# Kernel tuning notes

Measured on AMD Instinct MI355X. Metric: run time of the kernel, lower is better.

## Reference

```python
import jax, jax.numpy as jnp
import numpy as np

FP8_MAX = 448.0  # float8_e4m3fn max
NUM_HEADS = 16

def _fp8_quant_dequant(t):
    # per-(batch, head) symmetric scaling into fp8 e4m3 range, cast to fp8 and back
    amax = jnp.max(jnp.abs(t), axis=(-2, -1), keepdims=True)
    scale = FP8_MAX / jnp.maximum(amax, 1e-12)
    t8 = (t * scale).astype(jnp.float8_e4m3fn).astype(t.dtype)
    return t8 / scale

def setup_inputs() -> dict:
    key = jax.random.key(0)
    k1, k2, k3 = jax.random.split(key, 3)
    B, N, C = 2, 2048, 1024
    x = jax.random.normal(k1, (B, N, C), dtype=jnp.float32)
    w_qkv = jax.random.normal(k2, (C, 3 * C), dtype=jnp.float32) * (C ** -0.5)
    w_proj = jax.random.normal(k3, (C, C), dtype=jnp.float32) * (C ** -0.5)
    b_proj = jnp.zeros((C,), dtype=jnp.float32)
    return {"x": x, "w_qkv": w_qkv, "w_proj": w_proj, "b_proj": b_proj}

def reference(x, w_qkv, w_proj, b_proj):
    B, N, C = x.shape
    H = NUM_HEADS
    D = C // H
    scale = D ** -0.5
    qkv = (x @ w_qkv).reshape(B, N, 3, H, D).transpose(2, 0, 3, 1, 4)  # [3,B,H,N,D]
    q, k, v = qkv[0], qkv[1], qkv[2]
    # sage-style fp8 quantize/dequant of q and k fused into score computation
    q = _fp8_quant_dequant(q)
    k = _fp8_quant_dequant(k)
    scores = jnp.einsum('bhqd,bhkd->bhqk', q, k) * scale  # [B,H,N,N]
    causal = jnp.tril(jnp.ones((N, N), dtype=bool))
    scores = jnp.where(causal[None, None], scores, jnp.finfo(scores.dtype).min)
    attn = jax.nn.softmax(scores, axis=-1)
    out = jnp.einsum('bhqk,bhkd->bhqd', attn, v)  # [B,H,N,D]
    out = out.transpose(0, 2, 1, 3).reshape(B, N, C)
    return out @ w_proj + b_proj
```

## Files before the change

kernel.cpp:

```cpp
#include <hip/hip_runtime.h>

#define B_   2
#define N_   2048
#define C_   1024
#define H_   16
#define D_   64
#define BH_  (B_*H_)
#define NDH  (N_*D_)
#define M1   (B_*N_)

typedef __attribute__((ext_vector_type(4))) float    f32x4;
typedef __attribute__((ext_vector_type(8))) _Float16 f16x8;
typedef __attribute__((ext_vector_type(4))) _Float16 f16x4;

#define GLOAD_LDS(gp, lp) \
  __builtin_amdgcn_global_load_lds((const __attribute__((address_space(1))) void*)(gp), \
                                   (__attribute__((address_space(3))) void*)(lp), 16, 0, 0)

__global__ void k_cvt16(const float* __restrict__ in, _Float16* __restrict__ out, int n4) {
  int i = blockIdx.x * blockDim.x + threadIdx.x;
  if (i >= n4) return;
  float4 v = ((const float4*)in)[i];
  f16x4 o;
  o.x = (_Float16)v.x; o.y = (_Float16)v.y; o.z = (_Float16)v.z; o.w = (_Float16)v.w;
  ((f16x4*)out)[i] = o;
}

__global__ __launch_bounds__(256) void k_transmerge(const float* __restrict__ wq,
                                                    const float* __restrict__ wp,
                                                    _Float16* __restrict__ whT,
                                                    _Float16* __restrict__ wpT,
                                                    unsigned* __restrict__ amax_u) {
  if (blockIdx.x == 0 && threadIdx.x < 64) amax_u[threadIdx.x] = 0u;
  __shared__ _Float16 t[64][68];
  int idx = blockIdx.x;
  const float* in; _Float16* out; int Cc, cx, cy;
  if (idx < 768) { in = wq; out = whT; Cc = 3072; cx = idx % 48; cy = idx / 48; }
  else { idx -= 768; in = wp; out = wpT; Cc = 1024; cx = idx % 16; cy = idx / 16; }
  const int R = 1024;
  int c0 = cx * 64, r0 = cy * 64;
  int tid = threadIdx.x;
  int cq = tid & 15, rq = tid >> 4;
#pragma unroll
  for (int i = 0; i < 4; ++i) {
    int r = rq + i * 16;
    float4 v = *(const float4*)(in + (size_t)(r0 + r) * Cc + c0 + cq * 4);
    t[r][cq*4+0] = (_Float16)v.x;
    t[r][cq*4+1] = (_Float16)v.y;
    t[r][cq*4+2] = (_Float16)v.z;
    t[r][cq*4+3] = (_Float16)v.w;
  }
  __syncthreads();
#pragma unroll
  for (int i = 0; i < 4; ++i) {
    int c = rq + i * 16;
    f16x4 o;
    o.x = t[cq*4+0][c];
    o.y = t[cq*4+1][c];
    o.z = t[cq*4+2][c];
    o.w = t[cq*4+3][c];
    *(f16x4*)(out + (size_t)(c0 + c) * R + r0 + cq * 4) = o;
  }
}

__global__ __launch_bounds__(256) void k_gemm_qkv(const _Float16* __restrict__ A,
                                                  const _Float16* __restrict__ BT,
                                                  _Float16* __restrict__ qh,
                                                  _Float16* __restrict__ kh,
                                                  _Float16* __restrict__ vh,
                                                  unsigned* __restrict__ amax_u) {
  __shared__ __align__(16) _Float16 As[128 * 32];
  __shared__ __align__(16) _Float16 Bs[128 * 32];
  const int tid = threadIdx.x, lane = tid & 63, wave = tid >> 6;
  const int wm = wave >> 1, wn = wave & 1;
  const int mcol = lane & 15, quad = lane >> 4;
  const int m0 = blockIdx.x * 128, n0 = blockIdx.y * 128;
  f32x4 acc[4][4] = {};
  for (int k0 = 0; k0 < 1024; k0 += 32) {
#pragma unroll
    for (int r = 0; r < 2; ++r) {
      int c = tid + r * 256;
      int row = c >> 2, kc = c & 3;
      GLOAD_LDS(A  + (size_t)(m0 + row) * 1024 + k0 + kc * 8, &As[c * 8]);
      GLOAD_LDS(BT + (size_t)(n0 + row) * 1024 + k0 + kc * 8, &Bs[c * 8]);
    }
    __syncthreads();
    f16x8 af[4], bf[4];
#pragma unroll
    for (int tm = 0; tm < 4; ++tm)
      af[tm] = *(const f16x8*)&As[(wm * 64 + tm * 16 + mcol) * 32 + quad * 8];
#pragma unroll
    for (int tn = 0; tn < 4; ++tn)
      bf[tn] = *(const f16x8*)&Bs[(wn * 64 + tn * 16 + mcol) * 32 + quad * 8];
#pragma unroll
    for (int tm = 0; tm < 4; ++tm)
#pragma unroll
      for (int tn = 0; tn < 4; ++tn)
        acc[tm][tn] = __builtin_amdgcn_mfma_f32_16x16x32_f16(af[tm], bf[tn], acc[tm][tn], 0, 0, 0);
    __syncthreads();
  }
  const int sec = n0 >> 10;
  if (sec < 2) {
    _Float16* dst = sec ? kh : qh;
    float mxv = 0.f;
#pragma unroll
    for (int tm = 0; tm < 4; ++tm)
#pragma unroll
      for (int tn = 0; tn < 4; ++tn) {
        int rowb = m0 + wm * 64 + tm * 16 + quad * 4;
        int col = n0 + wn * 64 + tn * 16 + mcol;
        int cc = col & 1023, h = cc >> 6, d = cc & 63;
        int b = rowb >> 11, n = rowb & 2047;
        f32x4 a = acc[tm][tn];
        mxv = fmaxf(mxv, fmaxf(fmaxf(fabsf(a[0]), fabsf(a[1])),
                               fmaxf(fabsf(a[2]), fabsf(a[3]))));
        f16x4 o;
        o.x = (_Float16)a[0]; o.y = (_Float16)a[1];
        o.z = (_Float16)a[2]; o.w = (_Float16)a[3];
        *(f16x4*)&dst[(size_t)(b * 16 + h) * 131072 + (size_t)(n >> 5) * 2048 + d * 32 + (n & 31)] = o;
      }
#pragma unroll
    for (int off = 32; off; off >>= 1) mxv = fmaxf(mxv, __shfl_xor(mxv, off));
    if (lane == 0) {
      int head = ((n0 & 1023) >> 6) + wn;
      int plane = (m0 >> 11) * 16 + head;
      atomicMax(&amax_u[sec * 32 + plane], __float_as_uint(mxv));
    }
  } else {
#pragma unroll
    for (int tm = 0; tm < 4; ++tm)
#pragma unroll
      for (int tn = 0; tn < 4; ++tn) {
        int rowb = m0 + wm * 64 + tm * 16 + quad * 4;
        int col = n0 + wn * 64 + tn * 16 + mcol;
        int cc = col & 1023, h = cc >> 6, d = cc & 63;
        int b = rowb >> 11, n = rowb & 2047;
        f16x4 o;
        o.x = (_Float16)acc[tm][tn][0];
        o.y = (_Float16)acc[tm][tn][1];
        o.z = (_Float16)acc[tm][tn][2];
        o.w = (_Float16)acc[tm][tn][3];
        *(f16x4*)&vh[(size_t)(b * 16 + h) * 131072 + (size_t)(n >> 5) * 2048 + d * 32 + (n & 31)] = o;
      }
  }
}

__global__ __launch_bounds__(256) void k_quant(const _Float16* __restrict__ qh,
                                               const _Float16* __restrict__ kh,
                                               const float* __restrict__ amax,
                                               char* __restrict__ q8,
                                               char* __restrict__ k8) {
  __shared__ ushort T[32][72];
  int blk = blockIdx.x;
  int which = blk >> 11;
  int idx = blk & 2047;
  int bh = idx >> 6, chunk = idx & 63;
  const _Float16* src = (which ? kh : qh) + (size_t)bh * NDH + chunk * 2048;
  float s = 448.f / fmaxf(amax[which * 32 + bh], 1e-12f);
  int t = threadIdx.x;
  f16x8 v = *(const f16x8*)(src + t * 8);
  int d = t >> 2, kk0 = (t & 3) * 8;
#pragma unroll
  for (int j = 0; j < 8; ++j) T[kk0 + j][d] = ((const ushort*)&v)[j];
  __syncthreads();
  int r = t >> 3, d0 = (t & 7) * 8;
  f16x8 row = *(const f16x8*)&T[r][d0];
  float f[8];
#pragma unroll
  for (int j = 0; j < 8; ++j) f[j] = (float)((const _Float16*)&row)[j] * s;
  int lo = 0, hi = 0;
  lo = __builtin_amdgcn_cvt_pk_fp8_f32(f[0], f[1], lo, false);
  lo = __builtin_amdgcn_cvt_pk_fp8_f32(f[2], f[3], lo, true);
  hi = __builtin_amdgcn_cvt_pk_fp8_f32(f[4], f[5], hi, false);
  hi = __builtin_amdgcn_cvt_pk_fp8_f32(f[6], f[7], hi, true);
  int2 o; o.x = lo; o.y = hi;
  if (which == 0) {
    char* dst = q8 + (size_t)bh * NDH + (size_t)(chunk * 32 + r) * 64 + d0;
    *(int2*)dst = o;
  } else {
    int e = (r >> 2) & 1;
    int mc = (r >> 3) * 4 + (r & 3);
    int kb = d0 >> 5, dq = (d0 >> 3) & 3;
    char* dst = k8 + (size_t)bh * NDH + chunk * 2048 + (e * 2 + kb) * 512 + mc * 32 + dq * 8;
    *(int2*)dst = o;
  }
}

__global__ __launch_bounds__(256, 2) void k_flash(const char* __restrict__ q8,
                                                  const char* __restrict__ k8,
                                                  const _Float16* __restrict__ vh,
                                                  const float* __restrict__ amax,
                                                  _Float16* __restrict__ attn) {
  const int bh = blockIdx.x;
  const int wave = threadIdx.x >> 6, lane = threadIdx.x & 63;
  const int mcol = lane & 15, quad = lane >> 4;
  const int pr = blockIdx.y * 4 + wave;
  const int ga = pr, gb = 127 - pr;
  const int ta = (ga >> 3) + 1;

  float sq = 448.f / fmaxf(amax[bh], 1e-12f);
  float sk = 448.f / fmaxf(amax[32 + bh], 1e-12f);
  const float c2 = (1.f / (sq * sk)) * 0.125f * 1.44269504089f;

  const size_t pbase = (size_t)bh * NDH;
  const char* kbase = k8 + pbase + mcol * 32 + quad * 8;
  const _Float16* vbase = vh + pbase + mcol * 32 + quad * 8;
  const int qrowA = ga * 16 + mcol, qrowB = gb * 16 + mcol;
  long aqA0, aqA1, aqB0, aqB1;
  { const char* qp = q8 + pbase + (size_t)qrowA * 64;
    aqA0 = *(const long*)(qp + quad * 8); aqA1 = *(const long*)(qp + 32 + quad * 8); }
  { const char* qp = q8 + pbase + (size_t)qrowB * 64;
    aqB0 = *(const long*)(qp + quad * 8); aqB1 = *(const long*)(qp + 32 + quad * 8); }

  f32x4 O[4] = {};
  float m_i = -3e38f, l_i = 0.f;
  const int b = bh >> 4, h = bh & 15;
  const int kq = quad * 8;

  long kc[16], kn[16];
  {
    const char* kp = kbase;
#pragma unroll
    for (int i = 0; i < 16; ++i) kc[i] = *(const long*)(kp + i * 512);
  }

  auto body = [&](int t, long (&cur)[16], long (&nxt)[16]) {
    const bool inB = t >= ta;
    const int n0 = (inB ? t - ta : t) * 128;
    const long aq0 = inB ? aqB0 : aqA0;
    const long aq1 = inB ? aqB1 : aqA1;
    const int qrow = inB ? qrowB : qrowA;
    const bool last = inB ? (t == 16) : (t == ta - 1);

    f32x4 s[4][2];
#pragma unroll
    for (int p = 0; p < 4; ++p)
#pragma unroll
      for (int e = 0; e < 2; ++e) {
        f32x4 z = {};
        z = __builtin_amdgcn_mfma_f32_16x16x32_fp8_fp8(cur[p * 4 + e * 2 + 0], aq0, z, 0, 0, 0);
        z = __builtin_amdgcn_mfma_f32_16x16x32_fp8_fp8(cur[p * 4 + e * 2 + 1], aq1, z, 0, 0, 0);
        s[p][e] = z;
      }
    f16x8 va[4][4];
    {
      const _Float16* vp = vbase + (size_t)(n0 >> 5) * 2048;
#pragma unroll
      for (int p = 0; p < 4; ++p)
#pragma unroll
        for (int dt = 0; dt < 4; ++dt)
          va[dt][p] = *(const f16x8*)(vp + p * 2048 + dt * 512);
    }
    if (t < 16) {
      const int t2 = t + 1;
      const int n02 = ((t2 >= ta) ? t2 - ta : t2) * 128;
      const char* kp = kbase + (size_t)(n02 >> 5) * 2048;
#pragma unroll
      for (int i = 0; i < 16; ++i) nxt[i] = *(const long*)(kp + i * 512);
    }
    if (last) {
#pragma unroll
      for (int p = 0; p < 4; ++p)
#pragma unroll
        for (int e = 0; e < 2; ++e)
#pragma unroll
          for (int r = 0; r < 4; ++r) {
            int key = n0 + p * 32 + kq + e * 4 + r;
            float v = s[p][e][r] * c2;
            s[p][e][r] = (key <= qrow) ? v : -3e38f;
          }
    } else {
#pragma unroll
      for (int p = 0; p < 4; ++p)
#pragma unroll
        for (int e = 0; e < 2; ++e)
#pragma unroll
          for (int r = 0; r < 4; ++r)
            s[p][e][r] = s[p][e][r] * c2;
    }
    float fm[8];
#pragma unroll
    for (int p = 0; p < 4; ++p)
#pragma unroll
      for (int e = 0; e < 2; ++e) {
        f32x4 v = s[p][e];
        fm[p * 2 + e] = fmaxf(fmaxf(v[0], v[1]), fmaxf(v[2], v[3]));
      }
    float mx = fmaxf(fmaxf(fmaxf(fm[0], fm[1]), fmaxf(fm[2], fm[3])),
                     fmaxf(fmaxf(fm[4], fm[5]), fmaxf(fm[6], fm[7])));
    mx = fmaxf(mx, m_i);
    mx = fmaxf(mx, __shfl_xor(mx, 16));
    mx = fmaxf(mx, __shfl_xor(mx, 32));
    float alpha = exp2f(m_i - mx);
    m_i = mx;
    float fs[8];
#pragma unroll
    for (int p = 0; p < 4; ++p)
#pragma unroll
      for (int e = 0; e < 2; ++e) {
        float p0 = exp2f(s[p][e][0] - mx);
        float p1 = exp2f(s[p][e][1] - mx);
        float p2 = exp2f(s[p][e][2] - mx);
        float p3 = exp2f(s[p][e][3] - mx);
        s[p][e][0] = p0; s[p][e][1] = p1; s[p][e][2] = p2; s[p][e][3] = p3;
        fs[p * 2 + e] = (p0 + p1) + (p2 + p3);
      }
    float sum = ((fs[0] + fs[1]) + (fs[2] + fs[3])) + ((fs[4] + fs[5]) + (fs[6] + fs[7]));
    sum += __shfl_xor(sum, 16);
    sum += __shfl_xor(sum, 32);
    l_i = l_i * alpha + sum;
#pragma unroll
    for (int dt = 0; dt < 4; ++dt)
#pragma unroll
      for (int r = 0; r < 4; ++r)
        O[dt][r] *= alpha;
#pragma unroll
    for (int p = 0; p < 4; ++p) {
      f16x8 pb;
      pb[0] = (_Float16)s[p][0][0]; pb[1] = (_Float16)s[p][0][1];
      pb[2] = (_Float16)s[p][0][2]; pb[3] = (_Float16)s[p][0][3];
      pb[4] = (_Float16)s[p][1][0]; pb[5] = (_Float16)s[p][1][1];
      pb[6] = (_Float16)s[p][1][2]; pb[7] = (_Float16)s[p][1][3];
#pragma unroll
      for (int dt = 0; dt < 4; ++dt)
        O[dt] = __builtin_amdgcn_mfma_f32_16x16x32_f16(va[dt][p], pb, O[dt], 0, 0, 0);
    }
    if (last) {
      float rl = 1.f / l_i;
      _Float16* op = attn + ((size_t)b * 2048 + qrow) * 1024 + h * 64;
#pragma unroll
      for (int dt = 0; dt < 4; ++dt) {
        f16x4 o;
        o.x = (_Float16)(O[dt][0] * rl);
        o.y = (_Float16)(O[dt][1] * rl);
        o.z = (_Float16)(O[dt][2] * rl);
        o.w = (_Float16)(O[dt][3] * rl);
        *(f16x4*)(op + dt * 16 + quad * 4) = o;
        O[dt] = (f32x4){0.f, 0.f, 0.f, 0.f};
      }
      m_i = -3e38f; l_i = 0.f;
    }
  };

#pragma unroll 1
  for (int t = 0; t < 17; t += 2) {
    body(t, kc, kn);
    if (t + 1 < 17) body(t + 1, kn, kc);
  }
}

__global__ __launch_bounds__(256) void k_gemm_out(const _Float16* __restrict__ A,
                                                  const _Float16* __restrict__ BT,
                                                  const float* __restrict__ bias,
                                                  float* __restrict__ out) {
  __shared__ __align__(16) _Float16 As[128 * 32];
  __shared__ __align__(16) _Float16 Bs[128 * 32];
  const int tid = threadIdx.x, lane = tid & 63, wave = tid >> 6;
  const int wm = wave >> 1, wn = wave & 1;
  const int mcol = lane & 15, quad = lane >> 4;
  const int m0 = blockIdx.x * 128, n0 = blockIdx.y * 128;
  f32x4 acc[4][4] = {};
  for (int k0 = 0; k0 < 1024; k0 += 32) {
#pragma unroll
    for (int r = 0; r < 2; ++r) {
      int c = tid + r * 256;
      int row = c >> 2, kc = c & 3;
      GLOAD_LDS(A  + (size_t)(m0 + row) * 1024 + k0 + kc * 8, &As[c * 8]);
      GLOAD_LDS(BT + (size_t)(n0 + row) * 1024 + k0 + kc * 8, &Bs[c * 8]);
    }
    __syncthreads();
    f16x8 af[4], bf[4];
#pragma unroll
    for (int tm = 0; tm < 4; ++tm)
      af[tm] = *(const f16x8*)&As[(wm * 64 + tm * 16 + mcol) * 32 + quad * 8];
#pragma unroll
    for (int tn = 0; tn < 4; ++tn)
      bf[tn] = *(const f16x8*)&Bs[(wn * 64 + tn * 16 + mcol) * 32 + quad * 8];
#pragma unroll
    for (int tm = 0; tm < 4; ++tm)
#pragma unroll
      for (int tn = 0; tn < 4; ++tn)
        acc[tm][tn] = __builtin_amdgcn_mfma_f32_16x16x32_f16(af[tm], bf[tn], acc[tm][tn], 0, 0, 0);
    __syncthreads();
  }
#pragma unroll
  for (int tm = 0; tm < 4; ++tm)
#pragma unroll
    for (int tn = 0; tn < 4; ++tn)
#pragma unroll
      for (int reg = 0; reg < 4; ++reg) {
        int row = m0 + wm * 64 + tm * 16 + quad * 4 + reg;
        int col = n0 + wn * 64 + tn * 16 + mcol;
        out[(size_t)row * 1024 + col] = acc[tm][tn][reg] + bias[col];
      }
}

extern "C" void kernel_launch(void* const* d_in, const int* in_sizes, int n_in,
                              void* d_out, int out_size, void* d_ws, size_t ws_size,
                              hipStream_t stream) {
  const float* x      = (const float*)d_in[0];
  const float* w_qkv  = (const float*)d_in[1];
  const float* w_proj = (const float*)d_in[2];
  const float* b_proj = (const float*)d_in[3];
  float* out = (float*)d_out;

  char* ws = (char*)d_ws;
  _Float16* xh   = (_Float16*)ws; ws += (size_t)M1 * C_ * 2;
  _Float16* whT  = (_Float16*)ws; ws += (size_t)3 * C_ * C_ * 2;
  _Float16* wpT  = (_Float16*)ws; ws += (size_t)C_ * C_ * 2;
  _Float16* qh   = (_Float16*)ws; ws += (size_t)BH_ * NDH * 2;
  _Float16* kh   = (_Float16*)ws; ws += (size_t)BH_ * NDH * 2;
  _Float16* vh   = (_Float16*)ws; ws += (size_t)BH_ * NDH * 2;
  char*     q8   = (char*)ws;     ws += (size_t)BH_ * NDH;
  char*     k8   = (char*)ws;     ws += (size_t)BH_ * NDH;
  _Float16* attn = (_Float16*)ws; ws += (size_t)M1 * C_ * 2;
  float*    amx  = (float*)ws;    ws += 256;

  k_cvt16<<<(M1 * C_ / 4 + 255) / 256, 256, 0, stream>>>(x, xh, M1 * C_ / 4);
  k_transmerge<<<1024, 256, 0, stream>>>(w_qkv, w_proj, whT, wpT, (unsigned*)amx);
  k_gemm_qkv<<<dim3(M1 / 128, 3 * C_ / 128), 256, 0, stream>>>(xh, whT, qh, kh, vh, (unsigned*)amx);
  k_quant<<<4096, 256, 0, stream>>>(qh, kh, amx, q8, k8);
  k_flash<<<dim3(32, 16), 256, 0, stream>>>(q8, k8, vh, amx, attn);
  k_gemm_out<<<dim3(M1 / 128, C_ / 128), 256, 0, stream>>>(attn, wpT, b_proj, out);
}
```

Measured before the change: 215.4 us.

## Split each flash row-pair across two waves with LDS merge of partial softmax

The flash kernel now gives each pair of query tiles (A and B) to two waves instead of one. One wave does tile A plus the first part of tile B's keys, and the other does the rest of B's keys. The partial O, m and l are merged through shared memory. The grid doubles, launch bounds allow four blocks per CU, the score scale is folded into an fma before exp2, and P is packed with cvt_pkrtz. This aims to shorten the serial per-wave chain of 17 key tiles to 8–9 and raise occupancy, at the cost of LDS use, a __syncthreads, and more register pressure from the higher occupancy target.

```diff
diff --git a/kernel.cpp b/kernel.cpp
--- a/kernel.cpp
+++ b/kernel.cpp
@@ -12,6 +12,7 @@
 typedef __attribute__((ext_vector_type(4))) float    f32x4;
 typedef __attribute__((ext_vector_type(8))) _Float16 f16x8;
 typedef __attribute__((ext_vector_type(4))) _Float16 f16x4;
+typedef __attribute__((ext_vector_type(2))) __fp16   fp16v2;
 
 #define GLOAD_LDS(gp, lp) \
   __builtin_amdgcn_global_load_lds((const __attribute__((address_space(1))) void*)(gp), \
@@ -186,15 +187,18 @@
   }
 }
 
-__global__ __launch_bounds__(256, 2) void k_flash(const char* __restrict__ q8,
+__global__ __launch_bounds__(256, 4) void k_flash(const char* __restrict__ q8,
                                                   const char* __restrict__ k8,
                                                   const _Float16* __restrict__ vh,
                                                   const float* __restrict__ amax,
                                                   _Float16* __restrict__ attn) {
+  __shared__ float Osh[2][16][68];
+  __shared__ float Msh[2][16], Lsh[2][16];
   const int bh = blockIdx.x;
   const int wave = threadIdx.x >> 6, lane = threadIdx.x & 63;
   const int mcol = lane & 15, quad = lane >> 4;
-  const int pr = blockIdx.y * 4 + wave;
+  const int pi = wave >> 1, role = wave & 1;
+  const int pr = blockIdx.y * 2 + pi;
   const int ga = pr, gb = 127 - pr;
   const int ta = (ga >> 3) + 1;
 
@@ -206,31 +210,36 @@
   const char* kbase = k8 + pbase + mcol * 32 + quad * 8;
   const _Float16* vbase = vh + pbase + mcol * 32 + quad * 8;
   const int qrowA = ga * 16 + mcol, qrowB = gb * 16 + mcol;
-  long aqA0, aqA1, aqB0, aqB1;
-  { const char* qp = q8 + pbase + (size_t)qrowA * 64;
-    aqA0 = *(const long*)(qp + quad * 8); aqA1 = *(const long*)(qp + 32 + quad * 8); }
-  { const char* qp = q8 + pbase + (size_t)qrowB * 64;
-    aqB0 = *(const long*)(qp + quad * 8); aqB1 = *(const long*)(qp + 32 + quad * 8); }
+
+  long aq0v, aq1v;
+  { int qr = role ? qrowB : qrowA;
+    const char* qp = q8 + pbase + (size_t)qr * 64;
+    aq0v = *(const long*)(qp + quad * 8); aq1v = *(const long*)(qp + 32 + quad * 8); }
 
   f32x4 O[4] = {};
   float m_i = -3e38f, l_i = 0.f;
   const int b = bh >> 4, h = bh & 15;
   const int kq = quad * 8;
+  const int NT = role ? 8 : 9;
+
+  auto u_n0 = [&](int u) -> int {
+    if (role) return (9 - ta + u) << 7;
+    return (u < ta ? u : u - ta) << 7;
+  };
 
   long kc[16], kn[16];
   {
-    const char* kp = kbase;
+    const char* kp = kbase + (size_t)(u_n0(0) >> 5) * 2048;
 #pragma unroll
     for (int i = 0; i < 16; ++i) kc[i] = *(const long*)(kp + i * 512);
   }
 
-  auto body = [&](int t, long (&cur)[16], long (&nxt)[16]) {
-    const bool inB = t >= ta;
-    const int n0 = (inB ? t - ta : t) * 128;
-    const long aq0 = inB ? aqB0 : aqA0;
-    const long aq1 = inB ? aqB1 : aqA1;
-    const int qrow = inB ? qrowB : qrowA;
-    const bool last = inB ? (t == 16) : (t == ta - 1);
+  auto body = [&](int u, long (&cur)[16], long (&nxt)[16]) {
+    const bool inA = (!role) && (u < ta);
+    const int n0 = u_n0(u);
+    const int qrow = inA ? qrowA : qrowB;
+    const bool maskT = role ? (u == 7) : (u == ta - 1);
+    const bool emitA = (!role) && (u == ta - 1);
 
     f32x4 s[4][2];
 #pragma unroll
@@ -238,8 +247,8 @@
 #pragma unroll
       for (int e = 0; e < 2; ++e) {
         f32x4 z = {};
-        z = __builtin_amdgcn_mfma_f32_16x16x32_fp8_fp8(cur[p * 4 + e * 2 + 0], aq0, z, 0, 0, 0);
-        z = __builtin_amdgcn_mfma_f32_16x16x32_fp8_fp8(cur[p * 4 + e * 2 + 1], aq1, z, 0, 0, 0);
+        z = __builtin_amdgcn_mfma_f32_16x16x32_fp8_fp8(cur[p * 4 + e * 2 + 0], aq0v, z, 0, 0, 0);
+        z = __builtin_amdgcn_mfma_f32_16x16x32_fp8_fp8(cur[p * 4 + e * 2 + 1], aq1v, z, 0, 0, 0);
         s[p][e] = z;
       }
     f16x8 va[4][4];
@@ -251,14 +260,12 @@
         for (int dt = 0; dt < 4; ++dt)
           va[dt][p] = *(const f16x8*)(vp + p * 2048 + dt * 512);
     }
-    if (t < 16) {
-      const int t2 = t + 1;
-      const int n02 = ((t2 >= ta) ? t2 - ta : t2) * 128;
-      const char* kp = kbase + (size_t)(n02 >> 5) * 2048;
+    if (u + 1 < NT) {
+      const char* kp = kbase + (size_t)(u_n0(u + 1) >> 5) * 2048;
 #pragma unroll
       for (int i = 0; i < 16; ++i) nxt[i] = *(const long*)(kp + i * 512);
     }
-    if (last) {
+    if (maskT) {
 #pragma unroll
       for (int p = 0; p < 4; ++p)
 #pragma unroll
@@ -266,17 +273,8 @@
 #pragma unroll
           for (int r = 0; r < 4; ++r) {
             int key = n0 + p * 32 + kq + e * 4 + r;
-            float v = s[p][e][r] * c2;
-            s[p][e][r] = (key <= qrow) ? v : -3e38f;
+            s[p][e][r] = (key <= qrow) ? s[p][e][r] : -3e38f;
           }
-    } else {
-#pragma unroll
-      for (int p = 0; p < 4; ++p)
-#pragma unroll
-        for (int e = 0; e < 2; ++e)
-#pragma unroll
-          for (int r = 0; r < 4; ++r)
-            s[p][e][r] = s[p][e][r] * c2;
     }
     float fm[8];
 #pragma unroll
@@ -286,23 +284,25 @@
         f32x4 v = s[p][e];
         fm[p * 2 + e] = fmaxf(fmaxf(v[0], v[1]), fmaxf(v[2], v[3]));
       }
-    float mx = fmaxf(fmaxf(fmaxf(fm[0], fm[1]), fmaxf(fm[2], fm[3])),
+    float rm = fmaxf(fmaxf(fmaxf(fm[0], fm[1]), fmaxf(fm[2], fm[3])),
                      fmaxf(fmaxf(fm[4], fm[5]), fmaxf(fm[6], fm[7])));
-    mx = fmaxf(mx, m_i);
+    float mx = fmaxf(m_i, rm * c2);
     mx = fmaxf(mx, __shfl_xor(mx, 16));
     mx = fmaxf(mx, __shfl_xor(mx, 32));
     float alpha = exp2f(m_i - mx);
     m_i = mx;
     float fs[8];
+    union { f16x8 v8; fp16v2 v2[4]; } pb[4];
 #pragma unroll
     for (int p = 0; p < 4; ++p)
 #pragma unroll
       for (int e = 0; e < 2; ++e) {
-        float p0 = exp2f(s[p][e][0] - mx);
-        float p1 = exp2f(s[p][e][1] - mx);
-        float p2 = exp2f(s[p][e][2] - mx);
-        float p3 = exp2f(s[p][e][3] - mx);
-        s[p][e][0] = p0; s[p][e][1] = p1; s[p][e][2] = p2; s[p][e][3] = p3;
+        float p0 = exp2f(__builtin_fmaf(s[p][e][0], c2, -mx));
+        float p1 = exp2f(__builtin_fmaf(s[p][e][1], c2, -mx));
+        float p2 = exp2f(__builtin_fmaf(s[p][e][2], c2, -mx));
+        float p3 = exp2f(__builtin_fmaf(s[p][e][3], c2, -mx));
+        pb[p].v2[e * 2 + 0] = __builtin_amdgcn_cvt_pkrtz(p0, p1);
+        pb[p].v2[e * 2 + 1] = __builtin_amdgcn_cvt_pkrtz(p2, p3);
         fs[p * 2 + e] = (p0 + p1) + (p2 + p3);
       }
     float sum = ((fs[0] + fs[1]) + (fs[2] + fs[3])) + ((fs[4] + fs[5]) + (fs[6] + fs[7]));
@@ -315,19 +315,13 @@
       for (int r = 0; r < 4; ++r)
         O[dt][r] *= alpha;
 #pragma unroll
-    for (int p = 0; p < 4; ++p) {
-      f16x8 pb;
-      pb[0] = (_Float16)s[p][0][0]; pb[1] = (_Float16)s[p][0][1];
-      pb[2] = (_Float16)s[p][0][2]; pb[3] = (_Float16)s[p][0][3];
-      pb[4] = (_Float16)s[p][1][0]; pb[5] = (_Float16)s[p][1][1];
-      pb[6] = (_Float16)s[p][1][2]; pb[7] = (_Float16)s[p][1][3];
+    for (int p = 0; p < 4; ++p)
 #pragma unroll
       for (int dt = 0; dt < 4; ++dt)
-        O[dt] = __builtin_amdgcn_mfma_f32_16x16x32_f16(va[dt][p], pb, O[dt], 0, 0, 0);
-    }
-    if (last) {
+        O[dt] = __builtin_amdgcn_mfma_f32_16x16x32_f16(va[dt][p], pb[p].v8, O[dt], 0, 0, 0);
+    if (emitA) {
       float rl = 1.f / l_i;
-      _Float16* op = attn + ((size_t)b * 2048 + qrow) * 1024 + h * 64;
+      _Float16* op = attn + ((size_t)b * 2048 + qrowA) * 1024 + h * 64;
 #pragma unroll
       for (int dt = 0; dt < 4; ++dt) {
         f16x4 o;
@@ -339,13 +333,41 @@
         O[dt] = (f32x4){0.f, 0.f, 0.f, 0.f};
       }
       m_i = -3e38f; l_i = 0.f;
+      const char* qp = q8 + pbase + (size_t)qrowB * 64;
+      aq0v = *(const long*)(qp + quad * 8);
+      aq1v = *(const long*)(qp + 32 + quad * 8);
     }
   };
 
 #pragma unroll 1
-  for (int t = 0; t < 17; t += 2) {
-    body(t, kc, kn);
-    if (t + 1 < 17) body(t + 1, kn, kc);
+  for (int u = 0; u < NT; u += 2) {
+    body(u, kc, kn);
+    if (u + 1 < NT) body(u + 1, kn, kc);
+  }
+
+  if (role) {
+#pragma unroll
+    for (int dt = 0; dt < 4; ++dt)
+      *(f32x4*)&Osh[pi][mcol][dt * 16 + quad * 4] = O[dt];
+    if (quad == 0) { Msh[pi][mcol] = m_i; Lsh[pi][mcol] = l_i; }
+  }
+  __syncthreads();
+  if (!role) {
+    float m1 = Msh[pi][mcol], l1 = Lsh[pi][mcol];
+    float m = fmaxf(m_i, m1);
+    float a0 = exp2f(m_i - m), a1 = exp2f(m1 - m);
+    float rl = 1.f / (a0 * l_i + a1 * l1);
+    _Float16* op = attn + ((size_t)b * 2048 + qrowB) * 1024 + h * 64;
+#pragma unroll
+    for (int dt = 0; dt < 4; ++dt) {
+      f32x4 o1 = *(const f32x4*)&Osh[pi][mcol][dt * 16 + quad * 4];
+      f16x4 o;
+      o.x = (_Float16)((a0 * O[dt][0] + a1 * o1[0]) * rl);
+      o.y = (_Float16)((a0 * O[dt][1] + a1 * o1[1]) * rl);
+      o.z = (_Float16)((a0 * O[dt][2] + a1 * o1[2]) * rl);
+      o.w = (_Float16)((a0 * O[dt][3] + a1 * o1[3]) * rl);
+      *(f16x4*)(op + dt * 16 + quad * 4) = o;
+    }
   }
 }
 
@@ -420,6 +442,6 @@
   k_transmerge<<<1024, 256, 0, stream>>>(w_qkv, w_proj, whT, wpT, (unsigned*)amx);
   k_gemm_qkv<<<dim3(M1 / 128, 3 * C_ / 128), 256, 0, stream>>>(xh, whT, qh, kh, vh, (unsigned*)amx);
   k_quant<<<4096, 256, 0, stream>>>(qh, kh, amx, q8, k8);
-  k_flash<<<dim3(32, 16), 256, 0, stream>>>(q8, k8, vh, amx, attn);
+  k_flash<<<dim3(32, 32), 256, 0, stream>>>(q8, k8, vh, amx, attn);
   k_gemm_out<<<dim3(M1 / 128, C_ / 128), 256, 0, stream>>>(attn, wpT, b_proj, out);
 }
```

Measured after the change: 348.4 us. +61.8%, slower.
